# Optimization experiments

Measured on AMD Instinct MI355X. Metric: run time of the kernel, lower is better.

The kernel has to match this reference:

```python
import jax, jax.numpy as jnp
import numpy as np

EMBED_DIM = 1024
NUM_HEADS = 16
DEPTH = EMBED_DIM // NUM_HEADS
SCALE_FACTOR = 0.5
SEQ = 2048
BATCH = 2


def setup_inputs() -> dict:
    key = jax.random.key(0)
    ks = jax.random.split(key, 6)
    x = jax.random.normal(ks[0], (SEQ, BATCH, EMBED_DIM), dtype=jnp.float32)
    attn_mask = jnp.zeros((SEQ, SEQ), dtype=jnp.float32)
    key_padding_mask = jnp.zeros((BATCH, SEQ), dtype=bool)
    # Linear params (torch convention: y = x @ W.T + b)
    s_in = 1.0 / np.sqrt(EMBED_DIM)
    qkv_w = jax.random.uniform(ks[1], (3 * EMBED_DIM, EMBED_DIM), jnp.float32, -s_in, s_in)
    qkv_b = jax.random.uniform(ks[2], (3 * EMBED_DIM,), jnp.float32, -s_in, s_in)
    out_w = jax.random.uniform(ks[3], (EMBED_DIM, EMBED_DIM), jnp.float32, -s_in, s_in)
    out_b = jax.random.uniform(ks[4], (EMBED_DIM,), jnp.float32, -s_in, s_in)
    return {"x": x, "attn_mask": attn_mask, "key_padding_mask": key_padding_mask,
            "qkv_w": qkv_w, "qkv_b": qkv_b, "out_w": out_w, "out_b": out_b}


def reference(x, attn_mask, key_padding_mask, qkv_w, qkv_b, out_w, out_b):
    # x: [S, B, E] -> [B, S, E]
    xb = jnp.transpose(x, (1, 0, 2))
    B, S, E = xb.shape
    qkv = xb @ qkv_w.T + qkv_b                       # [B, S, 3E]
    q, k, v = jnp.split(qkv, 3, axis=2)
    def split_heads(t):                              # [B, S, E] -> [B, H, S, d]
        return jnp.transpose(t.reshape(B, S, NUM_HEADS, DEPTH), (0, 2, 1, 3))
    q, k, v = split_heads(q), split_heads(k), split_heads(v)
    scores = jnp.einsum('bhqd,bhkd->bhqk', q, k) / (DEPTH ** SCALE_FACTOR)
    scores = jnp.where(key_padding_mask[:, None, None, :], -jnp.inf, scores)
    scores = scores + attn_mask[None, None, :, :]
    attn = jax.nn.softmax(scores, axis=-1)           # [B, H, S, S] (dropout p=0)
    wa = jnp.einsum('bhqk,bhkd->bhqd', attn, v)      # [B, H, S, d]
    wa = jnp.transpose(wa, (0, 2, 1, 3)).reshape(B, S, E)
    out = wa @ out_w.T + out_b                       # [B, S, E]
    out = jnp.transpose(out, (1, 0, 2))              # [S, B, E]
    attn_mean = jnp.mean(attn, axis=1)               # [B, S, S]
    return out, attn_mean
```

## Files before the change

### kernel.cpp

```cpp
#include <hip/hip_runtime.h>
#include <hip/hip_bf16.h>


#define Sq 2048
#define Bb 2
#define Ee 1024
#define Hh 16
#define Dd 64
#define LOG2E 1.4426950408889634f
#define QSCALE 0.18033688011112042f

typedef __attribute__((ext_vector_type(8))) short bhalf8;
typedef __attribute__((ext_vector_type(4))) float f32x4;

__device__ __forceinline__ void gld16(const __hip_bfloat16* g, __hip_bfloat16* l) {
    __builtin_amdgcn_global_load_lds(
        (const __attribute__((address_space(1))) unsigned int*)g,
        (__attribute__((address_space(3))) unsigned int*)l, 16, 0, 0);
}

__device__ __forceinline__ int pkbf(float a, float b) {
    union { __hip_bfloat16 h[2]; int i; } u;
    u.h[0] = __float2bfloat16(a);
    u.h[1] = __float2bfloat16(b);
    return u.i;
}

__device__ __forceinline__ int tile_off(int s) {
    return ((s >> 2) & 1) * 2048 + (s >> 7) * 512 + (s & 3) * 128 + ((s >> 3) & 15) * 8;
}

__device__ __forceinline__ int swz(int t) {
    return (t & ~63) | ((t & 7) << 3) | ((t >> 3) & 7);
}

__device__ __forceinline__ int kperm(int p) {
    return (p & 3) | (((p >> 5) & 1) << 2) | ((p & 12) << 1) | (((p >> 4) & 1) << 5);
}

__global__ __launch_bounds__(256) void prep_k(
    const float* __restrict__ x, const float* __restrict__ am,
    const unsigned int* __restrict__ kpm32,
    const float* __restrict__ qkv_w, const float* __restrict__ out_w,
    __hip_bfloat16* __restrict__ xb, __hip_bfloat16* __restrict__ qwb,
    __hip_bfloat16* __restrict__ owb, unsigned int* __restrict__ flag)
{
    const long i = (long)blockIdx.x*256 + threadIdx.x;
    if (i < 1048576) {
        float4 v = ((const float4*)am)[i];
        bool nz = (v.x != 0.f) | (v.y != 0.f) | (v.z != 0.f) | (v.w != 0.f);
        if (i < 1024) nz |= (kpm32[i] != 0u);
        if (__ballot(nz)) { if ((threadIdx.x & 63) == 0) atomicOr(flag, 1u); }
    } else if (i < 2097152) {
        const long j = i - 1048576;
        const int m = (int)(j >> 8), e4 = (int)(j & 255);
        const int b = m >> 11, s = m & 2047;
        float4 v = ((const float4*)x)[(size_t)(s*Bb + b)*256 + e4];
        union { __hip_bfloat16 h[4]; uint2 u; } o;
        o.h[0]=__float2bfloat16(v.x); o.h[1]=__float2bfloat16(v.y);
        o.h[2]=__float2bfloat16(v.z); o.h[3]=__float2bfloat16(v.w);
        ((uint2*)xb)[(size_t)m*256 + e4] = o.u;
    } else if (i < 2883584) {
        const long j = i - 2097152;
        float4 v = ((const float4*)qkv_w)[j];
        union { __hip_bfloat16 h[4]; uint2 u; } o;
        o.h[0]=__float2bfloat16(v.x); o.h[1]=__float2bfloat16(v.y);
        o.h[2]=__float2bfloat16(v.z); o.h[3]=__float2bfloat16(v.w);
        ((uint2*)qwb)[j] = o.u;
    } else if (i < 3145728) {
        const long j = i - 2883584;
        float4 v = ((const float4*)out_w)[j];
        union { __hip_bfloat16 h[4]; uint2 u; } o;
        o.h[0]=__float2bfloat16(v.x); o.h[1]=__float2bfloat16(v.y);
        o.h[2]=__float2bfloat16(v.z); o.h[3]=__float2bfloat16(v.w);
        ((uint2*)owb)[j] = o.u;
    }
}

__global__ __launch_bounds__(256) void gemm_qkv(
    const __hip_bfloat16* __restrict__ A, const __hip_bfloat16* __restrict__ Bw,
    const float* __restrict__ bias,
    __hip_bfloat16* __restrict__ Qp, __hip_bfloat16* __restrict__ Kp,
    __hip_bfloat16* __restrict__ Vt)
{
    __shared__ __align__(16) __hip_bfloat16 As[128*32];
    __shared__ __align__(16) __hip_bfloat16 Bs[128*32];
    const int t = threadIdx.x;
    const int l = t & 63, lm = l & 15, quad = l >> 4;
    const int w = t >> 6;
    const int mw = (w & 1)*64, nw = (w >> 1)*64;
    const int m0 = blockIdx.y*128, n0 = blockIdx.x*128;

    const int srow = t >> 2;
    const int scol = (t & 3)*8;
    const __hip_bfloat16* ag = A  + (size_t)(m0 + srow)*1024 + scol;
    const __hip_bfloat16* bg = Bw + (size_t)(n0 + srow)*1024 + scol;
    __hip_bfloat16* al = As + t*8;
    __hip_bfloat16* bl = Bs + t*8;

    f32x4 acc[4][4] = {};
    for (int k0 = 0; k0 < 1024; k0 += 32) {
        __syncthreads();
        gld16(ag + k0, al);
        gld16(ag + (size_t)64*1024 + k0, al + 2048);
        gld16(bg + k0, bl);
        gld16(bg + (size_t)64*1024 + k0, bl + 2048);
        __syncthreads();
        bhalf8 af[4], bf[4];
#pragma unroll
        for (int i = 0; i < 4; i++) {
            af[i] = *(const bhalf8*)&As[(mw + i*16 + lm)*32 + quad*8];
            bf[i] = *(const bhalf8*)&Bs[(nw + i*16 + lm)*32 + quad*8];
        }
#pragma unroll
        for (int mf = 0; mf < 4; mf++)
#pragma unroll
            for (int nf = 0; nf < 4; nf++)
                acc[mf][nf] = __builtin_amdgcn_mfma_f32_16x16x32_bf16(af[mf], bf[nf], acc[mf][nf], 0,0,0);
    }
#pragma unroll
    for (int nf = 0; nf < 4; nf++) {
        const int n = n0 + nw + nf*16 + lm;
        const float bz = bias[n];
        const int which = n >> 10, hh = (n >> 6) & 15, dd = n & 63;
#pragma unroll
        for (int mf = 0; mf < 4; mf++)
#pragma unroll
            for (int r = 0; r < 4; r++) {
                const int m = m0 + mw + mf*16 + quad*4 + r;
                const int b2 = m >> 11, s2 = m & 2047;
                const float vf = acc[mf][nf][r] + bz;
                if (which == 0)
                    Qp[((size_t)(b2*Hh + hh)*Sq + s2)*Dd + dd] = __float2bfloat16(vf * QSCALE);
                else if (which == 1)
                    Kp[((size_t)(b2*Hh + hh)*Sq + s2)*Dd + dd] = __float2bfloat16(vf);
                else
                    Vt[((size_t)(b2*Hh + hh)*Dd + dd)*Sq + s2] = __float2bfloat16(vf);
            }
    }
}

__global__ __launch_bounds__(256, 4) void attn_mfma(
    const __hip_bfloat16* __restrict__ Qp, const __hip_bfloat16* __restrict__ Kp,
    const __hip_bfloat16* __restrict__ Vt,
    const float* __restrict__ am, const unsigned char* __restrict__ kpm,
    const unsigned int* __restrict__ flag,
    __hip_bfloat16* __restrict__ wa, float* __restrict__ rlbuf)
{
    __shared__ __align__(16) __hip_bfloat16 Ks[4096];
    __shared__ __align__(16) __hip_bfloat16 Vs[4096];
    const int t = threadIdx.x;
    const int w = t >> 6, l = t & 63, lm = l & 15, quad = l >> 4;
    const int blk = blockIdx.x;
    const int xcd = blk & 7;
    const int qt  = (blk >> 3) & 31;
    const int grp = blk >> 8;
    const int bh  = grp*8 + xcd;
    const int b   = bh >> 4, h = bh & 15;
    const int q   = qt*64 + w*16 + lm;
    const bool masked = (flag[0] != 0u);

    const __hip_bfloat16* qbase = Qp + (size_t)bh*Sq*Dd;
    const __hip_bfloat16* kbase = Kp + (size_t)bh*Sq*Dd;
    const __hip_bfloat16* vbase = Vt + (size_t)bh*Dd*Sq;

    bhalf8 bq[2];
    bq[0] = *(const bhalf8*)(qbase + (size_t)q*Dd + quad*8);
    bq[1] = *(const bhalf8*)(qbase + (size_t)q*Dd + quad*8 + 32);

    f32x4 o[4] = {};
    float lsum = 0.f;

    const int g0 = swz(t), g1 = g0 + 256;
    const int off0 = tile_off(g0), off1 = tile_off(g1);
    const int krow0 = kperm(g0 >> 3);
    const int krow1 = kperm(g1 >> 3);
    const int kcol  = (g0 & 7)*8;
    const int vrow0 = g0 >> 3, vrow1 = g1 >> 3;

    uint4 kreg0 = *(const uint4*)(kbase + (size_t)krow0*Dd + kcol);
    uint4 kreg1 = *(const uint4*)(kbase + (size_t)krow1*Dd + kcol);
    uint4 vreg0 = *(const uint4*)(vbase + (size_t)vrow0*Sq + kcol);
    uint4 vreg1 = *(const uint4*)(vbase + (size_t)vrow1*Sq + kcol);

    for (int kt = 0; kt < 32; kt++) {
        __syncthreads();
        *(uint4*)&Ks[off0] = kreg0;
        *(uint4*)&Ks[off1] = kreg1;
        *(uint4*)&Vs[off0] = vreg0;
        *(uint4*)&Vs[off1] = vreg1;
        if (kt < 31) {
            const int kn = (kt + 1)*64;
            kreg0 = *(const uint4*)(kbase + (size_t)(kn + krow0)*Dd + kcol);
            kreg1 = *(const uint4*)(kbase + (size_t)(kn + krow1)*Dd + kcol);
            vreg0 = *(const uint4*)(vbase + (size_t)vrow0*Sq + kn + kcol);
            vreg1 = *(const uint4*)(vbase + (size_t)vrow1*Sq + kn + kcol);
        }
        __syncthreads();

        const int k0 = kt*64;
        f32x4 s[4] = {};
#pragma unroll
        for (int f = 0; f < 2; f++) {
            bhalf8 ak[4];
#pragma unroll
            for (int j = 0; j < 4; j++)
                ak[j] = *(const bhalf8*)&Ks[f*2048 + j*512 + l*8];
#pragma unroll
            for (int j = 0; j < 4; j++)
                s[j] = __builtin_amdgcn_mfma_f32_16x16x32_bf16(ak[j], bq[f], s[j], 0,0,0);
        }

        int pk[4][2];
#pragma unroll
        for (int j = 0; j < 4; j++) {
            float p[4];
#pragma unroll
            for (int r = 0; r < 4; r++) {
                float sv = s[j][r];
                if (masked) {
                    const int key = k0 + 32*(j & 1) + 8*quad + 4*(j >> 1) + r;
                    const float km = kpm[b*Sq + key] ? -1e30f : 0.0f;
                    sv += (am[(size_t)q*Sq + key] + km) * LOG2E;
                }
                p[r] = exp2f(sv);
            }
            lsum += (p[0]+p[1]) + (p[2]+p[3]);
            pk[j][0] = pkbf(p[0], p[1]);
            pk[j][1] = pkbf(p[2], p[3]);
        }

#pragma unroll
        for (int ks = 0; ks < 2; ks++) {
            union { int i[4]; bhalf8 v; } bp;
            bp.i[0] = pk[ks][0];
            bp.i[1] = pk[ks][1];
            bp.i[2] = pk[ks + 2][0];
            bp.i[3] = pk[ks + 2][1];
            bhalf8 av[4];
#pragma unroll
            for (int nd = 0; nd < 4; nd++)
                av[nd] = *(const bhalf8*)&Vs[ks*2048 + nd*512 + l*8];
#pragma unroll
            for (int nd = 0; nd < 4; nd++)
                o[nd] = __builtin_amdgcn_mfma_f32_16x16x32_bf16(av[nd], bp.v, o[nd], 0,0,0);
        }
    }

    lsum += __shfl_xor(lsum, 16, 64);
    lsum += __shfl_xor(lsum, 32, 64);
    const float rl = 1.0f / lsum;
    if (quad == 0) rlbuf[(size_t)bh*Sq + q] = rl * 0.0625f;

#pragma unroll
    for (int nd = 0; nd < 4; nd++) {
        union { __hip_bfloat16 hx[4]; uint2 u; } ou;
#pragma unroll
        for (int r = 0; r < 4; r++) ou.hx[r] = __float2bfloat16(o[nd][r] * rl);
        *(uint2*)(wa + ((size_t)b*Sq + q)*Ee + h*Dd + nd*16 + quad*4) = ou.u;
    }
}

__global__ __launch_bounds__(256) void attn_mean_k(
    const __hip_bfloat16* __restrict__ Qp, const __hip_bfloat16* __restrict__ Kp,
    const float* __restrict__ am, const unsigned char* __restrict__ kpm,
    const unsigned int* __restrict__ flag,
    const float* __restrict__ rlbuf, float* __restrict__ attn_mean)
{
    __shared__ __align__(16) __hip_bfloat16 Ks[2][4096];
    const int t = threadIdx.x;
    const int w = t >> 6, l = t & 63, lm = l & 15, quad = l >> 4;
    const int blk = blockIdx.x;
    const int q0idx = (blk & 7) | (((blk >> 8) & 1) << 3);
    const int kc    = ((blk >> 3) & 31) * 64;
    const int b     = (blk >> 9) & 1;
    const int q0    = q0idx * 128;
    const bool masked = (flag[0] != 0u);

    const int g0 = swz(t), g1 = g0 + 256;
    const int off0 = tile_off(g0), off1 = tile_off(g1);
    const int qa = q0 + w*32;

    float macc[2][4][4] = {};
    uint4 kr0, kr1;

    {
        const __hip_bfloat16* kg = Kp + ((size_t)(b*Hh)*Sq + kc)*Dd;
        uint4 a0 = *(const uint4*)(kg + (size_t)g0*8);
        uint4 a1 = *(const uint4*)(kg + (size_t)g1*8);
        *(uint4*)&Ks[0][off0] = a0;
        *(uint4*)&Ks[0][off1] = a1;
        const __hip_bfloat16* kg1 = kg + (size_t)Sq*Dd;
        kr0 = *(const uint4*)(kg1 + (size_t)g0*8);
        kr1 = *(const uint4*)(kg1 + (size_t)g1*8);
    }

    for (int h = 0; h < Hh; h++) {
        __syncthreads();
        if (h < Hh - 1) {
            *(uint4*)&Ks[(h + 1) & 1][off0] = kr0;
            *(uint4*)&Ks[(h + 1) & 1][off1] = kr1;
            if (h < Hh - 2) {
                const __hip_bfloat16* kn = Kp + ((size_t)(b*Hh + h + 2)*Sq + kc)*Dd;
                kr0 = *(const uint4*)(kn + (size_t)g0*8);
                kr1 = *(const uint4*)(kn + (size_t)g1*8);
            }
        }

        const size_t base = (size_t)(b*Hh + h)*Sq;
        const __hip_bfloat16* Kc = Ks[h & 1];
#pragma unroll
        for (int su = 0; su < 2; su++) {
            const int qrow = qa + su*16;
            const __hip_bfloat16* qg = Qp + (base + qrow + lm)*Dd + quad*8;
            f32x4 s[4] = {};
#pragma unroll
            for (int f = 0; f < 2; f++) {
                bhalf8 aq = *(const bhalf8*)(qg + f*32);
#pragma unroll
                for (int j = 0; j < 4; j++) {
                    bhalf8 bk = *(const bhalf8*)&Kc[f*2048 + j*512 + l*8];
                    s[j] = __builtin_amdgcn_mfma_f32_16x16x32_bf16(aq, bk, s[j], 0,0,0);
                }
            }
            const f32x4 rl4 = *(const f32x4*)(rlbuf + base + qrow + quad*4);
#pragma unroll
            for (int j = 0; j < 4; j++)
#pragma unroll
                for (int r = 0; r < 4; r++) {
                    float sv = s[j][r];
                    if (masked) {
                        const int key = kc + j*16 + lm;
                        const float km = kpm[b*Sq + key] ? -1e30f : 0.0f;
                        sv += (am[(size_t)(qrow + quad*4 + r)*Sq + key] + km) * LOG2E;
                    }
                    macc[su][j][r] += exp2f(sv) * rl4[r];
                }
        }
    }

#pragma unroll
    for (int su = 0; su < 2; su++)
#pragma unroll
        for (int j = 0; j < 4; j++)
#pragma unroll
            for (int r = 0; r < 4; r++)
                attn_mean[((size_t)b*Sq + qa + su*16 + quad*4 + r)*Sq + kc + j*16 + lm] =
                    macc[su][j][r];
}

__global__ __launch_bounds__(256) void gemm_out(
    const __hip_bfloat16* __restrict__ A, const __hip_bfloat16* __restrict__ Bw,
    const float* __restrict__ bias, float* __restrict__ outp)
{
    __shared__ __align__(16) __hip_bfloat16 As[128*32];
    __shared__ __align__(16) __hip_bfloat16 Bs[128*32];
    const int t = threadIdx.x;
    const int l = t & 63, lm = l & 15, quad = l >> 4;
    const int w = t >> 6;
    const int mw = (w & 1)*64, nw = (w >> 1)*64;
    const int m0 = blockIdx.y*128, n0 = blockIdx.x*128;

    const int srow = t >> 2;
    const int scol = (t & 3)*8;
    const __hip_bfloat16* ag = A  + (size_t)(m0 + srow)*1024 + scol;
    const __hip_bfloat16* bg = Bw + (size_t)(n0 + srow)*1024 + scol;
    __hip_bfloat16* al = As + t*8;
    __hip_bfloat16* bl = Bs + t*8;

    f32x4 acc[4][4] = {};
    for (int k0 = 0; k0 < 1024; k0 += 32) {
        __syncthreads();
        gld16(ag + k0, al);
        gld16(ag + (size_t)64*1024 + k0, al + 2048);
        gld16(bg + k0, bl);
        gld16(bg + (size_t)64*1024 + k0, bl + 2048);
        __syncthreads();
        bhalf8 af[4], bf[4];
#pragma unroll
        for (int i = 0; i < 4; i++) {
            af[i] = *(const bhalf8*)&As[(mw + i*16 + lm)*32 + quad*8];
            bf[i] = *(const bhalf8*)&Bs[(nw + i*16 + lm)*32 + quad*8];
        }
#pragma unroll
        for (int mf = 0; mf < 4; mf++)
#pragma unroll
            for (int nf = 0; nf < 4; nf++)
                acc[mf][nf] = __builtin_amdgcn_mfma_f32_16x16x32_bf16(af[mf], bf[nf], acc[mf][nf], 0,0,0);
    }
#pragma unroll
    for (int nf = 0; nf < 4; nf++) {
        const int n = n0 + nw + nf*16 + lm;
        const float bz = bias[n];
#pragma unroll
        for (int mf = 0; mf < 4; mf++)
#pragma unroll
            for (int r = 0; r < 4; r++) {
                const int m = m0 + mw + mf*16 + quad*4 + r;
                const int b2 = m >> 11, s2 = m & 2047;
                outp[((size_t)s2*Bb + b2)*Ee + n] = acc[mf][nf][r] + bz;
            }
    }
}

extern "C" void kernel_launch(void* const* d_in, const int* in_sizes, int n_in,
                              void* d_out, int out_size, void* d_ws, size_t ws_size,
                              hipStream_t stream) {
    const float*         x         = (const float*)d_in[0];
    const float*         attn_mask = (const float*)d_in[1];
    const unsigned char* kpm       = (const unsigned char*)d_in[2];
    const float*         qkv_w     = (const float*)d_in[3];
    const float*         qkv_b     = (const float*)d_in[4];
    const float*         out_w     = (const float*)d_in[5];
    const float*         out_b     = (const float*)d_in[6];

    float* outp      = (float*)d_out;
    float* attn_mean = outp + 4194304;

    __hip_bfloat16* xb  = (__hip_bfloat16*)d_ws;
    __hip_bfloat16* qwb = xb  + 4194304;
    __hip_bfloat16* owb = qwb + 3145728;
    __hip_bfloat16* Qp  = owb + 1048576;
    __hip_bfloat16* Kp  = Qp  + 4194304;
    __hip_bfloat16* Vt  = Kp  + 4194304;
    __hip_bfloat16* wab = Vt  + 4194304;
    float* rlbuf        = (float*)(wab + 4194304);
    unsigned int* flag  = (unsigned int*)(rlbuf + 65536);

    hipMemsetAsync(flag, 0, sizeof(unsigned int), stream);
    prep_k<<<12288, 256, 0, stream>>>(x, attn_mask, (const unsigned int*)kpm,
                                      qkv_w, out_w, xb, qwb, owb, flag);
    gemm_qkv<<<dim3(24, 32), 256, 0, stream>>>(xb, qwb, qkv_b, Qp, Kp, Vt);
    attn_mfma<<<dim3(1024), 256, 0, stream>>>(Qp, Kp, Vt, attn_mask, kpm, flag, wab, rlbuf);
    attn_mean_k<<<dim3(1024), 256, 0, stream>>>(Qp, Kp, attn_mask, kpm, flag, rlbuf, attn_mean);
    gemm_out<<<dim3(8, 32), 256, 0, stream>>>(wab, owb, out_b, outp);
}
```

Before: 308.0 us.

## Double-buffer K/V LDS tiles in attention, add setprio, use packed bf16 convert

The attention kernel now keeps two LDS buffers for K and V and prefetches two tiles ahead, so each iteration needs one barrier instead of two and the LDS stores overlap the MFMA work. MFMA regions are wrapped in s_setprio to favour matrix issue across waves. bf16 packing now uses the hardware v_cvt_pk_bf16_f32 instruction in the prep kernel and the attention epilogue. LDS use doubles, which could lower occupancy under the launch bound of 4 blocks per CU. The packed convert may round differently from __float2bfloat16.

Result: no change. 312.1 us (+1.4%).

```diff
diff --git a/kernel.cpp b/kernel.cpp
--- a/kernel.cpp
+++ b/kernel.cpp
@@ -20,10 +20,9 @@
 }
 
 __device__ __forceinline__ int pkbf(float a, float b) {
-    union { __hip_bfloat16 h[2]; int i; } u;
-    u.h[0] = __float2bfloat16(a);
-    u.h[1] = __float2bfloat16(b);
-    return u.i;
+    int r;
+    asm("v_cvt_pk_bf16_f32 %0, %1, %2" : "=v"(r) : "v"(a), "v"(b));
+    return r;
 }
 
 __device__ __forceinline__ int tile_off(int s) {
@@ -56,24 +55,24 @@
         const int m = (int)(j >> 8), e4 = (int)(j & 255);
         const int b = m >> 11, s = m & 2047;
         float4 v = ((const float4*)x)[(size_t)(s*Bb + b)*256 + e4];
-        union { __hip_bfloat16 h[4]; uint2 u; } o;
-        o.h[0]=__float2bfloat16(v.x); o.h[1]=__float2bfloat16(v.y);
-        o.h[2]=__float2bfloat16(v.z); o.h[3]=__float2bfloat16(v.w);
-        ((uint2*)xb)[(size_t)m*256 + e4] = o.u;
+        uint2 o;
+        o.x = (unsigned)pkbf(v.x, v.y);
+        o.y = (unsigned)pkbf(v.z, v.w);
+        ((uint2*)xb)[(size_t)m*256 + e4] = o;
     } else if (i < 2883584) {
         const long j = i - 2097152;
         float4 v = ((const float4*)qkv_w)[j];
-        union { __hip_bfloat16 h[4]; uint2 u; } o;
-        o.h[0]=__float2bfloat16(v.x); o.h[1]=__float2bfloat16(v.y);
-        o.h[2]=__float2bfloat16(v.z); o.h[3]=__float2bfloat16(v.w);
-        ((uint2*)qwb)[j] = o.u;
+        uint2 o;
+        o.x = (unsigned)pkbf(v.x, v.y);
+        o.y = (unsigned)pkbf(v.z, v.w);
+        ((uint2*)qwb)[j] = o;
     } else if (i < 3145728) {
         const long j = i - 2883584;
         float4 v = ((const float4*)out_w)[j];
-        union { __hip_bfloat16 h[4]; uint2 u; } o;
-        o.h[0]=__float2bfloat16(v.x); o.h[1]=__float2bfloat16(v.y);
-        o.h[2]=__float2bfloat16(v.z); o.h[3]=__float2bfloat16(v.w);
-        ((uint2*)owb)[j] = o.u;
+        uint2 o;
+        o.x = (unsigned)pkbf(v.x, v.y);
+        o.y = (unsigned)pkbf(v.z, v.w);
+        ((uint2*)owb)[j] = o;
     }
 }
 
@@ -147,8 +146,8 @@
     const unsigned int* __restrict__ flag,
     __hip_bfloat16* __restrict__ wa, float* __restrict__ rlbuf)
 {
-    __shared__ __align__(16) __hip_bfloat16 Ks[4096];
-    __shared__ __align__(16) __hip_bfloat16 Vs[4096];
+    __shared__ __align__(16) __hip_bfloat16 Ks[2][4096];
+    __shared__ __align__(16) __hip_bfloat16 Vs[2][4096];
     const int t = threadIdx.x;
     const int w = t >> 6, l = t & 63, lm = l & 15, quad = l >> 4;
     const int blk = blockIdx.x;
@@ -178,38 +177,52 @@
     const int kcol  = (g0 & 7)*8;
     const int vrow0 = g0 >> 3, vrow1 = g1 >> 3;
 
-    uint4 kreg0 = *(const uint4*)(kbase + (size_t)krow0*Dd + kcol);
-    uint4 kreg1 = *(const uint4*)(kbase + (size_t)krow1*Dd + kcol);
-    uint4 vreg0 = *(const uint4*)(vbase + (size_t)vrow0*Sq + kcol);
-    uint4 vreg1 = *(const uint4*)(vbase + (size_t)vrow1*Sq + kcol);
+    {
+        uint4 a0 = *(const uint4*)(kbase + (size_t)krow0*Dd + kcol);
+        uint4 a1 = *(const uint4*)(kbase + (size_t)krow1*Dd + kcol);
+        uint4 a2 = *(const uint4*)(vbase + (size_t)vrow0*Sq + kcol);
+        uint4 a3 = *(const uint4*)(vbase + (size_t)vrow1*Sq + kcol);
+        *(uint4*)&Ks[0][off0] = a0;
+        *(uint4*)&Ks[0][off1] = a1;
+        *(uint4*)&Vs[0][off0] = a2;
+        *(uint4*)&Vs[0][off1] = a3;
+    }
+    uint4 kreg0 = *(const uint4*)(kbase + (size_t)(64 + krow0)*Dd + kcol);
+    uint4 kreg1 = *(const uint4*)(kbase + (size_t)(64 + krow1)*Dd + kcol);
+    uint4 vreg0 = *(const uint4*)(vbase + (size_t)vrow0*Sq + 64 + kcol);
+    uint4 vreg1 = *(const uint4*)(vbase + (size_t)vrow1*Sq + 64 + kcol);
 
     for (int kt = 0; kt < 32; kt++) {
         __syncthreads();
-        *(uint4*)&Ks[off0] = kreg0;
-        *(uint4*)&Ks[off1] = kreg1;
-        *(uint4*)&Vs[off0] = vreg0;
-        *(uint4*)&Vs[off1] = vreg1;
+        const int cur = kt & 1, nxt = cur ^ 1;
         if (kt < 31) {
-            const int kn = (kt + 1)*64;
-            kreg0 = *(const uint4*)(kbase + (size_t)(kn + krow0)*Dd + kcol);
-            kreg1 = *(const uint4*)(kbase + (size_t)(kn + krow1)*Dd + kcol);
-            vreg0 = *(const uint4*)(vbase + (size_t)vrow0*Sq + kn + kcol);
-            vreg1 = *(const uint4*)(vbase + (size_t)vrow1*Sq + kn + kcol);
-        }
-        __syncthreads();
+            *(uint4*)&Ks[nxt][off0] = kreg0;
+            *(uint4*)&Ks[nxt][off1] = kreg1;
+            *(uint4*)&Vs[nxt][off0] = vreg0;
+            *(uint4*)&Vs[nxt][off1] = vreg1;
+            if (kt < 30) {
+                const int kn = (kt + 2)*64;
+                kreg0 = *(const uint4*)(kbase + (size_t)(kn + krow0)*Dd + kcol);
+                kreg1 = *(const uint4*)(kbase + (size_t)(kn + krow1)*Dd + kcol);
+                vreg0 = *(const uint4*)(vbase + (size_t)vrow0*Sq + kn + kcol);
+                vreg1 = *(const uint4*)(vbase + (size_t)vrow1*Sq + kn + kcol);
+            }
+        }
 
         const int k0 = kt*64;
         f32x4 s[4] = {};
+        __builtin_amdgcn_s_setprio(1);
 #pragma unroll
         for (int f = 0; f < 2; f++) {
             bhalf8 ak[4];
 #pragma unroll
             for (int j = 0; j < 4; j++)
-                ak[j] = *(const bhalf8*)&Ks[f*2048 + j*512 + l*8];
+                ak[j] = *(const bhalf8*)&Ks[cur][f*2048 + j*512 + l*8];
 #pragma unroll
             for (int j = 0; j < 4; j++)
                 s[j] = __builtin_amdgcn_mfma_f32_16x16x32_bf16(ak[j], bq[f], s[j], 0,0,0);
         }
+        __builtin_amdgcn_s_setprio(0);
 
         int pk[4][2];
 #pragma unroll
@@ -230,6 +243,7 @@
             pk[j][1] = pkbf(p[2], p[3]);
         }
 
+        __builtin_amdgcn_s_setprio(1);
 #pragma unroll
         for (int ks = 0; ks < 2; ks++) {
             union { int i[4]; bhalf8 v; } bp;
@@ -240,11 +254,12 @@
             bhalf8 av[4];
 #pragma unroll
             for (int nd = 0; nd < 4; nd++)
-                av[nd] = *(const bhalf8*)&Vs[ks*2048 + nd*512 + l*8];
+                av[nd] = *(const bhalf8*)&Vs[cur][ks*2048 + nd*512 + l*8];
 #pragma unroll
             for (int nd = 0; nd < 4; nd++)
                 o[nd] = __builtin_amdgcn_mfma_f32_16x16x32_bf16(av[nd], bp.v, o[nd], 0,0,0);
         }
+        __builtin_amdgcn_s_setprio(0);
     }
 
     lsum += __shfl_xor(lsum, 16, 64);
@@ -254,10 +269,10 @@
 
 #pragma unroll
     for (int nd = 0; nd < 4; nd++) {
-        union { __hip_bfloat16 hx[4]; uint2 u; } ou;
-#pragma unroll
-        for (int r = 0; r < 4; r++) ou.hx[r] = __float2bfloat16(o[nd][r] * rl);
-        *(uint2*)(wa + ((size_t)b*Sq + q)*Ee + h*Dd + nd*16 + quad*4) = ou.u;
+        uint2 ou;
+        ou.x = (unsigned)pkbf(o[nd][0] * rl, o[nd][1] * rl);
+        ou.y = (unsigned)pkbf(o[nd][2] * rl, o[nd][3] * rl);
+        *(uint2*)(wa + ((size_t)b*Sq + q)*Ee + h*Dd + nd*16 + quad*4) = ou;
     }
 }
 
```

## Merge attn-mean and output GEMM into one launch; use packed bf16 conversion

Applied to the files above, without the earlier changes.

The output projection GEMM and the attention-mean kernel are combined into a single launch, with the first 256 blocks doing the GEMM and the rest computing attn_mean, sharing one LDS buffer. This removes one kernel launch and lets the two independent tail stages run concurrently on the GPU instead of back to back. Separately, float-to-bf16 packing now uses the v_cvt_pk_bf16_f32 instruction via inline asm in place of per-element conversions. The merged kernel's LDS and register footprint is the larger of the two, which may lower occupancy for the attn-mean blocks.

After: 308.1 us. About the same (+0.1%).

```diff
diff --git a/kernel.cpp b/kernel.cpp
--- a/kernel.cpp
+++ b/kernel.cpp
@@ -20,10 +20,9 @@
 }
 
 __device__ __forceinline__ int pkbf(float a, float b) {
-    union { __hip_bfloat16 h[2]; int i; } u;
-    u.h[0] = __float2bfloat16(a);
-    u.h[1] = __float2bfloat16(b);
-    return u.i;
+    int r;
+    asm("v_cvt_pk_bf16_f32 %0, %1, %2" : "=v"(r) : "v"(a), "v"(b));
+    return r;
 }
 
 __device__ __forceinline__ int tile_off(int s) {
@@ -56,24 +55,24 @@
         const int m = (int)(j >> 8), e4 = (int)(j & 255);
         const int b = m >> 11, s = m & 2047;
         float4 v = ((const float4*)x)[(size_t)(s*Bb + b)*256 + e4];
-        union { __hip_bfloat16 h[4]; uint2 u; } o;
-        o.h[0]=__float2bfloat16(v.x); o.h[1]=__float2bfloat16(v.y);
-        o.h[2]=__float2bfloat16(v.z); o.h[3]=__float2bfloat16(v.w);
-        ((uint2*)xb)[(size_t)m*256 + e4] = o.u;
+        uint2 o;
+        o.x = (unsigned)pkbf(v.x, v.y);
+        o.y = (unsigned)pkbf(v.z, v.w);
+        ((uint2*)xb)[(size_t)m*256 + e4] = o;
     } else if (i < 2883584) {
         const long j = i - 2097152;
         float4 v = ((const float4*)qkv_w)[j];
-        union { __hip_bfloat16 h[4]; uint2 u; } o;
-        o.h[0]=__float2bfloat16(v.x); o.h[1]=__float2bfloat16(v.y);
-        o.h[2]=__float2bfloat16(v.z); o.h[3]=__float2bfloat16(v.w);
-        ((uint2*)qwb)[j] = o.u;
+        uint2 o;
+        o.x = (unsigned)pkbf(v.x, v.y);
+        o.y = (unsigned)pkbf(v.z, v.w);
+        ((uint2*)qwb)[j] = o;
     } else if (i < 3145728) {
         const long j = i - 2883584;
         float4 v = ((const float4*)out_w)[j];
-        union { __hip_bfloat16 h[4]; uint2 u; } o;
-        o.h[0]=__float2bfloat16(v.x); o.h[1]=__float2bfloat16(v.y);
-        o.h[2]=__float2bfloat16(v.z); o.h[3]=__float2bfloat16(v.w);
-        ((uint2*)owb)[j] = o.u;
+        uint2 o;
+        o.x = (unsigned)pkbf(v.x, v.y);
+        o.y = (unsigned)pkbf(v.z, v.w);
+        ((uint2*)owb)[j] = o;
     }
 }
 
@@ -254,23 +253,77 @@
 
 #pragma unroll
     for (int nd = 0; nd < 4; nd++) {
-        union { __hip_bfloat16 hx[4]; uint2 u; } ou;
-#pragma unroll
-        for (int r = 0; r < 4; r++) ou.hx[r] = __float2bfloat16(o[nd][r] * rl);
-        *(uint2*)(wa + ((size_t)b*Sq + q)*Ee + h*Dd + nd*16 + quad*4) = ou.u;
-    }
-}
-
-__global__ __launch_bounds__(256) void attn_mean_k(
+        uint2 ou;
+        ou.x = (unsigned)pkbf(o[nd][0] * rl, o[nd][1] * rl);
+        ou.y = (unsigned)pkbf(o[nd][2] * rl, o[nd][3] * rl);
+        *(uint2*)(wa + ((size_t)b*Sq + q)*Ee + h*Dd + nd*16 + quad*4) = ou;
+    }
+}
+
+__global__ __launch_bounds__(256) void tail_k(
     const __hip_bfloat16* __restrict__ Qp, const __hip_bfloat16* __restrict__ Kp,
     const float* __restrict__ am, const unsigned char* __restrict__ kpm,
     const unsigned int* __restrict__ flag,
-    const float* __restrict__ rlbuf, float* __restrict__ attn_mean)
+    const float* __restrict__ rlbuf, float* __restrict__ attn_mean,
+    const __hip_bfloat16* __restrict__ A, const __hip_bfloat16* __restrict__ Bw,
+    const float* __restrict__ bias, float* __restrict__ outp)
 {
-    __shared__ __align__(16) __hip_bfloat16 Ks[2][4096];
+    __shared__ __align__(16) __hip_bfloat16 sh[8192];
     const int t = threadIdx.x;
-    const int w = t >> 6, l = t & 63, lm = l & 15, quad = l >> 4;
-    const int blk = blockIdx.x;
+    const int l = t & 63, lm = l & 15, quad = l >> 4;
+    const int w = t >> 6;
+
+    if (blockIdx.x < 256) {
+        __hip_bfloat16* As = sh;
+        __hip_bfloat16* Bs = sh + 4096;
+        const int mw = (w & 1)*64, nw = (w >> 1)*64;
+        const int n0 = (blockIdx.x & 7)*128, m0 = (blockIdx.x >> 3)*128;
+
+        const int srow = t >> 2;
+        const int scol = (t & 3)*8;
+        const __hip_bfloat16* ag = A  + (size_t)(m0 + srow)*1024 + scol;
+        const __hip_bfloat16* bg = Bw + (size_t)(n0 + srow)*1024 + scol;
+        __hip_bfloat16* al = As + t*8;
+        __hip_bfloat16* bl = Bs + t*8;
+
+        f32x4 acc[4][4] = {};
+        for (int k0 = 0; k0 < 1024; k0 += 32) {
+            __syncthreads();
+            gld16(ag + k0, al);
+            gld16(ag + (size_t)64*1024 + k0, al + 2048);
+            gld16(bg + k0, bl);
+            gld16(bg + (size_t)64*1024 + k0, bl + 2048);
+            __syncthreads();
+            bhalf8 af[4], bf[4];
+#pragma unroll
+            for (int i = 0; i < 4; i++) {
+                af[i] = *(const bhalf8*)&As[(mw + i*16 + lm)*32 + quad*8];
+                bf[i] = *(const bhalf8*)&Bs[(nw + i*16 + lm)*32 + quad*8];
+            }
+#pragma unroll
+            for (int mf = 0; mf < 4; mf++)
+#pragma unroll
+                for (int nf = 0; nf < 4; nf++)
+                    acc[mf][nf] = __builtin_amdgcn_mfma_f32_16x16x32_bf16(af[mf], bf[nf], acc[mf][nf], 0,0,0);
+        }
+#pragma unroll
+        for (int nf = 0; nf < 4; nf++) {
+            const int n = n0 + nw + nf*16 + lm;
+            const float bz = bias[n];
+#pragma unroll
+            for (int mf = 0; mf < 4; mf++)
+#pragma unroll
+                for (int r = 0; r < 4; r++) {
+                    const int m = m0 + mw + mf*16 + quad*4 + r;
+                    const int b2 = m >> 11, s2 = m & 2047;
+                    outp[((size_t)s2*Bb + b2)*Ee + n] = acc[mf][nf][r] + bz;
+                }
+        }
+        return;
+    }
+
+    __hip_bfloat16 (*Ks)[4096] = (__hip_bfloat16(*)[4096])sh;
+    const int blk = blockIdx.x - 256;
     const int q0idx = (blk & 7) | (((blk >> 8) & 1) << 3);
     const int kc    = ((blk >> 3) & 31) * 64;
     const int b     = (blk >> 9) & 1;
@@ -349,60 +402,6 @@
                     macc[su][j][r];
 }
 
-__global__ __launch_bounds__(256) void gemm_out(
-    const __hip_bfloat16* __restrict__ A, const __hip_bfloat16* __restrict__ Bw,
-    const float* __restrict__ bias, float* __restrict__ outp)
-{
-    __shared__ __align__(16) __hip_bfloat16 As[128*32];
-    __shared__ __align__(16) __hip_bfloat16 Bs[128*32];
-    const int t = threadIdx.x;
-    const int l = t & 63, lm = l & 15, quad = l >> 4;
-    const int w = t >> 6;
-    const int mw = (w & 1)*64, nw = (w >> 1)*64;
-    const int m0 = blockIdx.y*128, n0 = blockIdx.x*128;
-
-    const int srow = t >> 2;
-    const int scol = (t & 3)*8;
-    const __hip_bfloat16* ag = A  + (size_t)(m0 + srow)*1024 + scol;
-    const __hip_bfloat16* bg = Bw + (size_t)(n0 + srow)*1024 + scol;
-    __hip_bfloat16* al = As + t*8;
-    __hip_bfloat16* bl = Bs + t*8;
-
-    f32x4 acc[4][4] = {};
-    for (int k0 = 0; k0 < 1024; k0 += 32) {
-        __syncthreads();
-        gld16(ag + k0, al);
-        gld16(ag + (size_t)64*1024 + k0, al + 2048);
-        gld16(bg + k0, bl);
-        gld16(bg + (size_t)64*1024 + k0, bl + 2048);
-        __syncthreads();
-        bhalf8 af[4], bf[4];
-#pragma unroll
-        for (int i = 0; i < 4; i++) {
-            af[i] = *(const bhalf8*)&As[(mw + i*16 + lm)*32 + quad*8];
-            bf[i] = *(const bhalf8*)&Bs[(nw + i*16 + lm)*32 + quad*8];
-        }
-#pragma unroll
-        for (int mf = 0; mf < 4; mf++)
-#pragma unroll
-            for (int nf = 0; nf < 4; nf++)
-                acc[mf][nf] = __builtin_amdgcn_mfma_f32_16x16x32_bf16(af[mf], bf[nf], acc[mf][nf], 0,0,0);
-    }
-#pragma unroll
-    for (int nf = 0; nf < 4; nf++) {
-        const int n = n0 + nw + nf*16 + lm;
-        const float bz = bias[n];
-#pragma unroll
-        for (int mf = 0; mf < 4; mf++)
-#pragma unroll
-            for (int r = 0; r < 4; r++) {
-                const int m = m0 + mw + mf*16 + quad*4 + r;
-                const int b2 = m >> 11, s2 = m & 2047;
-                outp[((size_t)s2*Bb + b2)*Ee + n] = acc[mf][nf][r] + bz;
-            }
-    }
-}
-
 extern "C" void kernel_launch(void* const* d_in, const int* in_sizes, int n_in,
                               void* d_out, int out_size, void* d_ws, size_t ws_size,
                               hipStream_t stream) {
@@ -432,6 +431,6 @@
                                       qkv_w, out_w, xb, qwb, owb, flag);
     gemm_qkv<<<dim3(24, 32), 256, 0, stream>>>(xb, qwb, qkv_b, Qp, Kp, Vt);
     attn_mfma<<<dim3(1024), 256, 0, stream>>>(Qp, Kp, Vt, attn_mask, kpm, flag, wab, rlbuf);
-    attn_mean_k<<<dim3(1024), 256, 0, stream>>>(Qp, Kp, attn_mask, kpm, flag, rlbuf, attn_mean);
-    gemm_out<<<dim3(8, 32), 256, 0, stream>>>(wab, owb, out_b, outp);
-}
+    tail_k<<<dim3(1280), 256, 0, stream>>>(Qp, Kp, attn_mask, kpm, flag, rlbuf, attn_mean,
+                                           wab, owb, out_b, outp);
+}
```
